# Kernel tuning notes

Measured on AMD Instinct MI355X. Metric: run time of the kernel, lower is better.

## Reference

```python
import jax, jax.numpy as jnp
import numpy as np

B, D, H, O, RH, P = 8192, 784, 2048, 1024, 128, 64
NI = NJ = NK = 4  # input regions / hidden groups / output groups


def _make_groups():
    idx = np.arange(28 * 28).reshape(28, 28)
    input_groups = np.stack([
        idx[:14, :14].ravel(), idx[:14, 14:].ravel(),
        idx[14:, :14].ravel(), idx[14:, 14:].ravel(),
    ]).astype(np.int32)                                   # [4, 196]
    hidden_groups = np.arange(H, dtype=np.int32).reshape(NJ, H // NJ)   # [4, 512]
    output_groups = np.arange(O, dtype=np.int32).reshape(NK, O // NK)   # [4, 256]
    return input_groups, hidden_groups, output_groups


def setup_inputs() -> dict:
    key = jax.random.key(0)
    ks = jax.random.split(key, 9)
    ig, hg, og = _make_groups()
    inp = {
        "x":   jax.random.normal(ks[0], (B, D), jnp.float32),
        "W1":  jax.random.normal(ks[1], (H, D), jnp.float32) / np.sqrt(D),
        "b1":  jax.random.normal(ks[2], (H,), jnp.float32) * 0.01,
        "W2":  jax.random.normal(ks[3], (O, H), jnp.float32) / np.sqrt(H),
        "b2":  jax.random.normal(ks[4], (O,), jnp.float32) * 0.01,
        "Wr1": jax.random.normal(ks[5], (RH, D), jnp.float32) / np.sqrt(D),
        "br1": jax.random.normal(ks[6], (RH,), jnp.float32) * 0.01,
        "Wr2": jax.random.normal(ks[7], (P, RH), jnp.float32) / np.sqrt(RH),
        "br2": jax.random.normal(ks[8], (P,), jnp.float32) * 0.01,
        "input_groups": jnp.asarray(ig),
        "hidden_groups": jnp.asarray(hg),
        "output_groups": jnp.asarray(og),
        "top_k": 8,
    }
    return inp


def reference(x, W1, b1, W2, b2, Wr1, br1, Wr2, br2,
              input_groups, hidden_groups, output_groups, top_k):
    # --- router MLP (eval mode: dropout = identity, no routing noise) ---
    h_r = jax.nn.relu(x @ Wr1.T + br1)
    scores = h_r @ Wr2.T + br2                      # [B, P]
    probs = jax.nn.softmax(scores, axis=-1)         # temperature = 1.0

    # --- top-k pathway selection + renormalization ---
    top_vals, top_idx = jax.lax.top_k(probs, top_k)
    bsz = x.shape[0]
    mask = jnp.zeros_like(probs).at[jnp.arange(bsz)[:, None], top_idx].set(top_vals)
    wts = mask / (mask.sum(axis=-1, keepdims=True) + 1e-8)
    wts4 = wts.reshape(bsz, NI, NJ, NK)             # pathway_idx = i*16 + j*4 + k

    # --- gather pathway sub-blocks ---
    x_reg = x[:, input_groups]                      # [B, I, 196]
    # W1g[i, j] = W1[hidden_groups[j]][:, input_groups[i]] -> [I, J, 512, 196]
    W1g = W1[hidden_groups[None, :, :, None], input_groups[:, None, None, :]]
    b1g = b1[hidden_groups]                         # [J, 512]
    # W2g[j, k] = W2[output_groups[k]][:, hidden_groups[j]] -> [J, K, 256, 512]
    W2g = W2[output_groups[None, :, :, None], hidden_groups[:, None, None, :]]
    b2g = b2[output_groups]                         # [K, 256]

    # --- pathway computation (exact erf GELU, as torch F.gelu default) ---
    hidden = jax.nn.gelu(
        jnp.einsum('bin,ijhn->ijbh', x_reg, W1g) + b1g[None, :, None, :],
        approximate=False)                          # [I, J, B, 512]
    # weighted pathway outputs, contracted over i, j, h without materializing
    # the full [I, J, K, B, 256] tensor
    out_main = jnp.einsum('ijbh,jkoh,bijk->bko', hidden, W2g, wts4)  # [B, K, 256]
    wsum = wts4.sum(axis=(1, 2))                    # [B, K] (bias weighted per pathway)
    out_blocks = out_main + wsum[:, :, None] * b2g[None]

    out = jnp.zeros((bsz, O), x.dtype).at[:, output_groups].add(out_blocks)
    return out
```

## Files before the change

### kernel.cpp

```cpp
#include <hip/hip_runtime.h>
#include <hip/hip_bf16.h>
#include <hip/hip_fp16.h>

#define B_  8192
#define D_  784
#define H_  2048
#define O_  1024
#define RH_ 128
#define P_  64
#define KP  224
#define KC  196

typedef __attribute__((ext_vector_type(8))) short short8;
typedef __attribute__((ext_vector_type(4))) float f32x4;

__device__ inline float bf2f(unsigned short u) {
  union { unsigned int i; float f; } v; v.i = ((unsigned int)u) << 16; return v.f;
}
__device__ inline unsigned short f2bf(float f) {
  __hip_bfloat16 h = __float2bfloat16(f);
  return *reinterpret_cast<unsigned short*>(&h);
}
__device__ inline unsigned short f2h(float f) {
  __half h = __float2half(f);
  return *reinterpret_cast<unsigned short*>(&h);
}
__device__ inline float h2f(unsigned short u) {
  __half h = *reinterpret_cast<__half*>(&u);
  return __half2float(h);
}
__device__ inline float erf_fast(float x) {
  float ax = fabsf(x);
  float t = 1.0f / (1.0f + 0.3275911f * ax);
  float p = ((((1.061405429f * t - 1.453152027f) * t + 1.421413741f) * t
              - 0.284496736f) * t + 0.254829592f) * t;
  float y = 1.0f - p * __expf(-ax * ax);
  return x < 0.f ? -y : y;
}
__device__ inline float gelu_exact(float v) {
  return 0.5f * v * (1.0f + erf_fast(v * 0.70710678118654752f));
}

__device__ inline void gload_lds16(const void* g, void* l) {
  __builtin_amdgcn_global_load_lds((const __attribute__((address_space(1))) void*)g,
                                   (__attribute__((address_space(3))) void*)l, 16, 0, 0);
}

__device__ inline void gemm128_bt(const unsigned short* __restrict__ A,
                                  const unsigned short* __restrict__ Bm,
                                  int K, unsigned short* smem, f32x4 acc[4][4]) {
  const int t = threadIdx.x;
  const int w = t >> 6, l = t & 63;
  const int wr = (w >> 1) * 64, wc = (w & 1) * 64;
  const int lr = l & 15;
  const int swr = (lr >> 1) & 3;
  const int s_orig = (t & 3) ^ ((t >> 3) & 3);
  const size_t srcOff = (size_t)(t >> 2) * K + s_orig * 8;
  const unsigned short* gA = A + srcOff;
  const unsigned short* gB = Bm + srcOff;
  char* lds = (char*)smem;
  char* ldsT = lds + t * 16;
  const int arow = (wr + lr) * 64 + (((l >> 4) ^ swr) * 16);
  const int brow = 8192 + (wc + lr) * 64 + (((l >> 4) ^ swr) * 16);
  const size_t halfA = (size_t)64 * K;
  for (int kt = 0; kt < K; kt += 32) {
    gload_lds16(gA + kt,         ldsT);
    gload_lds16(gA + kt + halfA, ldsT + 4096);
    gload_lds16(gB + kt,         ldsT + 8192);
    gload_lds16(gB + kt + halfA, ldsT + 12288);
    __syncthreads();
    short8 af[4], bfr[4];
#pragma unroll
    for (int f = 0; f < 4; ++f) {
      af[f]  = *(const short8*)(lds + arow + f * 1024);
      bfr[f] = *(const short8*)(lds + brow + f * 1024);
    }
#pragma unroll
    for (int fm = 0; fm < 4; ++fm)
#pragma unroll
      for (int fn = 0; fn < 4; ++fn)
        acc[fm][fn] = __builtin_amdgcn_mfma_f32_16x16x32_bf16(af[fm], bfr[fn], acc[fm][fn], 0, 0, 0);
    __syncthreads();
  }
}

__global__ void k_prep(const float* __restrict__ x, const float* __restrict__ W1,
                       const float* __restrict__ W2, const int* __restrict__ ig,
                       unsigned short* __restrict__ xreg, unsigned short* __restrict__ w1g,
                       unsigned short* __restrict__ w2b) {
  const size_t N1 = (size_t)4 * B_ * KP;
  const size_t N2 = (size_t)4 * H_ * KP;
  const size_t N3 = (size_t)O_ * H_;
  const size_t TOT = N1 + N2 + N3;
  for (size_t idx = (size_t)blockIdx.x * blockDim.x + threadIdx.x; idx < TOT;
       idx += (size_t)gridDim.x * blockDim.x) {
    if (idx < N1) {
      int n = (int)(idx % KP); size_t r = idx / KP;
      int b = (int)(r % B_); int i = (int)(r / B_);
      float v = (n < 196) ? x[(size_t)b * D_ + ig[i * 196 + n]] : 0.f;
      xreg[idx] = f2bf(v);
    } else if (idx < N1 + N2) {
      size_t q = idx - N1;
      int n = (int)(q % KP); size_t r = q / KP;
      int h = (int)(r % H_); int i = (int)(r / H_);
      float v = (n < 196) ? W1[(size_t)h * D_ + ig[i * 196 + n]] : 0.f;
      w1g[q] = f2bf(v);
    } else {
      size_t q = idx - N1 - N2;
      w2b[q] = f2bf(W2[q]);
    }
  }
}

__global__ __launch_bounds__(256) void k_r1s(const float* __restrict__ x,
    const float* __restrict__ Wr1, const float* __restrict__ br1,
    float* __restrict__ hrp) {
  __shared__ float As[64][33];
  __shared__ float Bs[64][33];
  const int b0 = blockIdx.x * 64;
  const int h0 = blockIdx.y * 64;
  const int kb = blockIdx.z * KC;
  const int kend = kb + KC;
  const int t = threadIdx.x;
  const int srow = t >> 2;
  const int scol = (t & 3) * 8;
  const int ty = t >> 4, tx = t & 15;
  float acc[4][4];
#pragma unroll
  for (int i = 0; i < 4; ++i)
#pragma unroll
    for (int j = 0; j < 4; ++j) acc[i][j] = 0.f;
  const float* gA = x   + (size_t)(b0 + srow) * D_;
  const float* gB = Wr1 + (size_t)(h0 + srow) * D_;
  for (int k0 = kb; k0 < kend; k0 += 32) {
    float4 a0 = (k0 + scol + 4  <= kend) ? *(const float4*)(gA + k0 + scol)     : float4{0,0,0,0};
    float4 a1 = (k0 + scol + 8  <= kend) ? *(const float4*)(gA + k0 + scol + 4) : float4{0,0,0,0};
    float4 w0 = (k0 + scol + 4  <= kend) ? *(const float4*)(gB + k0 + scol)     : float4{0,0,0,0};
    float4 w1 = (k0 + scol + 8  <= kend) ? *(const float4*)(gB + k0 + scol + 4) : float4{0,0,0,0};
    __syncthreads();
    *(float4*)&As[srow][scol]     = a0;
    *(float4*)&As[srow][scol + 4] = a1;
    *(float4*)&Bs[srow][scol]     = w0;
    *(float4*)&Bs[srow][scol + 4] = w1;
    __syncthreads();
#pragma unroll
    for (int kk = 0; kk < 8; ++kk) {
      float4 a4[4], b4[4];
#pragma unroll
      for (int i = 0; i < 4; ++i) a4[i] = *(const float4*)&As[ty * 4 + i][kk * 4];
#pragma unroll
      for (int j = 0; j < 4; ++j) b4[j] = *(const float4*)&Bs[tx * 4 + j][kk * 4];
#pragma unroll
      for (int i = 0; i < 4; ++i)
#pragma unroll
        for (int j = 0; j < 4; ++j)
          acc[i][j] += a4[i].x * b4[j].x + a4[i].y * b4[j].y +
                       a4[i].z * b4[j].z + a4[i].w * b4[j].w;
    }
  }
  float* hz = hrp + (size_t)blockIdx.z * B_ * RH_;
#pragma unroll
  for (int j = 0; j < 4; ++j) {
    const int h = h0 + tx * 4 + j;
    const float bias = (blockIdx.z == 0) ? br1[h] : 0.f;
#pragma unroll
    for (int i = 0; i < 4; ++i)
      hz[(size_t)(b0 + ty * 4 + i) * RH_ + h] = acc[i][j] + bias;
  }
}

#define R2S 32
__global__ __launch_bounds__(256) void k_r2(const float* __restrict__ hrp,
    const float* __restrict__ Wr2, const float* __restrict__ br2,
    float* __restrict__ wts, float* __restrict__ wsum) {
  __shared__ float Ws[64][130];
  __shared__ float hs[R2S][128];
  const int s0 = blockIdx.x * R2S;
  const int t = threadIdx.x;
  for (int idx = t; idx < 2048; idx += 256) {
    int r = idx >> 5, c = (idx & 31) * 4;
    *(float4*)&Ws[r][c] = *(const float4*)(Wr2 + (size_t)r * RH_ + c);
  }
  for (int idx = t; idx < R2S * 32; idx += 256) {
    int r = idx >> 5, c = (idx & 31) * 4;
    const size_t off = (size_t)(s0 + r) * RH_ + c;
    float4 p0 = *(const float4*)(hrp + off);
    float4 p1 = *(const float4*)(hrp + (size_t)1 * B_ * RH_ + off);
    float4 p2 = *(const float4*)(hrp + (size_t)2 * B_ * RH_ + off);
    float4 p3 = *(const float4*)(hrp + (size_t)3 * B_ * RH_ + off);
    float4 s;
    s.x = fmaxf(p0.x + p1.x + p2.x + p3.x, 0.f);
    s.y = fmaxf(p0.y + p1.y + p2.y + p3.y, 0.f);
    s.z = fmaxf(p0.z + p1.z + p2.z + p3.z, 0.f);
    s.w = fmaxf(p0.w + p1.w + p2.w + p3.w, 0.f);
    *(float4*)&hs[r][c] = s;
  }
  __syncthreads();
  const int w = t >> 6, p = t & 63;
  const float wb2 = br2[p];
  for (int si = 0; si < R2S / 4; ++si) {
    const int sl = w * (R2S / 4) + si;
    float sc = wb2;
#pragma unroll
    for (int kk = 0; kk < 32; ++kk) {
      float4 h4 = *(const float4*)&hs[sl][kk * 4];
      float4 w4 = *(const float4*)&Ws[p][kk * 4];
      sc += h4.x * w4.x + h4.y * w4.y + h4.z * w4.z + h4.w * w4.w;
    }
    float m = sc;
#pragma unroll
    for (int o = 32; o; o >>= 1) m = fmaxf(m, __shfl_xor(m, o));
    float e = __expf(sc - m);
    float Z = e;
#pragma unroll
    for (int o = 32; o; o >>= 1) Z += __shfl_xor(Z, o);
    bool sel = false;
    float ssum = 0.f;
    for (int it = 0; it < 8; ++it) {
      float v = sel ? -1.f : e;
      float vm = v;
#pragma unroll
      for (int o = 32; o; o >>= 1) vm = fmaxf(vm, __shfl_xor(vm, o));
      unsigned long long mask = __ballot(!sel && v == vm);
      int first = __ffsll((long long)mask) - 1;
      if (p == first) sel = true;
      ssum += vm;
    }
    const float dn = 1.0f / (ssum + 1e-8f * Z);
    const float wv = sel ? e * dn : 0.f;
    wts[(size_t)(s0 + sl) * 64 + p] = wv;
    float part = wv;
#pragma unroll
    for (int o = 4; o < 64; o <<= 1) part += __shfl_xor(part, o);
    if (p < 4) wsum[(size_t)(s0 + sl) * 4 + p] = part;
  }
}

__global__ __launch_bounds__(256) void k_l1(const unsigned short* __restrict__ xreg,
    const unsigned short* __restrict__ w1g, const float* __restrict__ b1,
    unsigned short* __restrict__ hid16) {
  __shared__ __align__(128) unsigned short smem[8192];
  const int mt = blockIdx.x, nt = blockIdx.y, iq = blockIdx.z;
  const unsigned short* A  = xreg + ((size_t)iq * B_ + mt * 128) * KP;
  const unsigned short* Bm = w1g + ((size_t)iq * H_ + nt * 128) * KP;
  f32x4 acc[4][4];
#pragma unroll
  for (int a = 0; a < 4; ++a)
#pragma unroll
    for (int b = 0; b < 4; ++b) acc[a][b] = (f32x4){0.f, 0.f, 0.f, 0.f};
  gemm128_bt(A, Bm, KP, smem, acc);
  const int t = threadIdx.x, w = t >> 6, l = t & 63;
  const int rbase = mt * 128 + (w >> 1) * 64 + (l >> 4) * 4;
  const int cbase = nt * 128 + (w & 1) * 64 + (l & 15);
#pragma unroll
  for (int fn = 0; fn < 4; ++fn) {
    const int n = cbase + fn * 16;
    const float bias = b1[n];
#pragma unroll
    for (int fm = 0; fm < 4; ++fm)
#pragma unroll
      for (int r = 0; r < 4; ++r) {
        const int m = rbase + fm * 16 + r;
        hid16[((size_t)iq * B_ + m) * H_ + n] = f2h(acc[fm][fn][r] + bias);
      }
  }
}

__global__ __launch_bounds__(256) void k_combine(unsigned short* __restrict__ hid,
                                                 const float* __restrict__ wts) {
  const int b = blockIdx.x;
  const int n = threadIdx.x * 8;
  const int j = n >> 9;
  const float* wb = wts + (size_t)b * 64;
  float g[4][8];
#pragma unroll
  for (int i = 0; i < 4; ++i) {
    short8 raw = *(const short8*)(hid + ((size_t)i * B_ + b) * H_ + n);
#pragma unroll
    for (int e = 0; e < 8; ++e) g[i][e] = gelu_exact(h2f((unsigned short)raw[e]));
  }
  short8 outv[4];
#pragma unroll
  for (int k = 0; k < 4; ++k) {
    const float w0 = wb[0 + j * 4 + k], w1 = wb[16 + j * 4 + k];
    const float w2 = wb[32 + j * 4 + k], w3 = wb[48 + j * 4 + k];
#pragma unroll
    for (int e = 0; e < 8; ++e) {
      float sv = g[0][e] * w0 + g[1][e] * w1 + g[2][e] * w2 + g[3][e] * w3;
      outv[k][e] = (short)f2bf(sv);
    }
  }
#pragma unroll
  for (int k = 0; k < 4; ++k)
    *(short8*)(hid + ((size_t)k * B_ + b) * H_ + n) = outv[k];
}

__global__ __launch_bounds__(256) void k_l2(const unsigned short* __restrict__ G,
    const unsigned short* __restrict__ w2b, const float* __restrict__ b2,
    const float* __restrict__ wsum, float* __restrict__ out) {
  __shared__ __align__(128) unsigned short smem[8192];
  const int mt = blockIdx.x, nt = blockIdx.y, k = blockIdx.z;
  const unsigned short* A  = G + ((size_t)k * B_ + mt * 128) * H_;
  const unsigned short* Bm = w2b + ((size_t)(k * 256 + nt * 128)) * H_;
  f32x4 acc[4][4];
#pragma unroll
  for (int a = 0; a < 4; ++a)
#pragma unroll
    for (int b = 0; b < 4; ++b) acc[a][b] = (f32x4){0.f, 0.f, 0.f, 0.f};
  gemm128_bt(A, Bm, H_, smem, acc);
  const int t = threadIdx.x, w = t >> 6, l = t & 63;
  const int rbase = mt * 128 + (w >> 1) * 64 + (l >> 4) * 4;
  const int cb = nt * 128 + (w & 1) * 64 + (l & 15);
#pragma unroll
  for (int fn = 0; fn < 4; ++fn) {
    const int ncol = k * 256 + cb + fn * 16;
    const float bias = b2[ncol];
#pragma unroll
    for (int fm = 0; fm < 4; ++fm)
#pragma unroll
      for (int r = 0; r < 4; ++r) {
        const int m = rbase + fm * 16 + r;
        out[(size_t)m * O_ + ncol] = acc[fm][fn][r] + wsum[m * 4 + k] * bias;
      }
  }
}

extern "C" void kernel_launch(void* const* d_in, const int* in_sizes, int n_in,
                              void* d_out, int out_size, void* d_ws, size_t ws_size,
                              hipStream_t stream) {
  const float* x   = (const float*)d_in[0];
  const float* W1  = (const float*)d_in[1];
  const float* b1  = (const float*)d_in[2];
  const float* W2  = (const float*)d_in[3];
  const float* b2  = (const float*)d_in[4];
  const float* Wr1 = (const float*)d_in[5];
  const float* br1 = (const float*)d_in[6];
  const float* Wr2 = (const float*)d_in[7];
  const float* br2 = (const float*)d_in[8];
  const int*   ig  = (const int*)d_in[9];
  float* out = (float*)d_out;
  char* ws = (char*)d_ws;
  unsigned short* xreg = (unsigned short*)(ws);
  unsigned short* w1g  = (unsigned short*)(ws + 14680064);
  unsigned short* w2b  = (unsigned short*)(ws + 18350080);
  float*          wts  = (float*)(ws + 22544384);
  float*          wsum = (float*)(ws + 24641536);
  unsigned short* hid  = (unsigned short*)(ws + 24772608);
  float*          hrp  = (float*)(ws + 24772608);

  k_prep<<<dim3(2048), dim3(256), 0, stream>>>(x, W1, W2, ig, xreg, w1g, w2b);
  k_r1s<<<dim3(B_ / 64, RH_ / 64, 4), dim3(256), 0, stream>>>(x, Wr1, br1, hrp);
  k_r2<<<dim3(B_ / R2S), dim3(256), 0, stream>>>(hrp, Wr2, br2, wts, wsum);
  k_l1<<<dim3(B_ / 128, H_ / 128, 4), dim3(256), 0, stream>>>(xreg, w1g, b1, hid);
  k_combine<<<dim3(B_), dim3(256), 0, stream>>>(hid, wts);
  k_l2<<<dim3(B_ / 128, 2, 4), dim3(256), 0, stream>>>(hid, w2b, b2, wsum, out);
}
```

Before: 253.5 us.

## Skip inactive (input-region, hidden-group) pathways in layer-1 GEMM via compacted row lists

Adds a compaction kernel that builds, for each (i,j) pair, a list of batch rows whose top-k routing weights are nonzero. The layer-1 GEMM then gathers only those rows, scatters its results back, and exits early for tiles beyond the active count. The combine kernel also skips reading and GELU for inactive i. The lists live temporarily in the output buffer, and the extra launch plus gathered loads add overhead.

```diff
diff --git a/kernel.cpp b/kernel.cpp
--- a/kernel.cpp
+++ b/kernel.cpp
@@ -46,28 +46,23 @@
                                    (__attribute__((address_space(3))) void*)l, 16, 0, 0);
 }
 
-__device__ inline void gemm128_bt(const unsigned short* __restrict__ A,
-                                  const unsigned short* __restrict__ Bm,
-                                  int K, unsigned short* smem, f32x4 acc[4][4]) {
+__device__ inline void gemm128_g(const unsigned short* gA0, const unsigned short* gA1,
+                                 const unsigned short* gB0, const unsigned short* gB1,
+                                 int K, unsigned short* smem, f32x4 acc[4][4]) {
   const int t = threadIdx.x;
   const int w = t >> 6, l = t & 63;
   const int wr = (w >> 1) * 64, wc = (w & 1) * 64;
   const int lr = l & 15;
   const int swr = (lr >> 1) & 3;
-  const int s_orig = (t & 3) ^ ((t >> 3) & 3);
-  const size_t srcOff = (size_t)(t >> 2) * K + s_orig * 8;
-  const unsigned short* gA = A + srcOff;
-  const unsigned short* gB = Bm + srcOff;
   char* lds = (char*)smem;
   char* ldsT = lds + t * 16;
   const int arow = (wr + lr) * 64 + (((l >> 4) ^ swr) * 16);
   const int brow = 8192 + (wc + lr) * 64 + (((l >> 4) ^ swr) * 16);
-  const size_t halfA = (size_t)64 * K;
   for (int kt = 0; kt < K; kt += 32) {
-    gload_lds16(gA + kt,         ldsT);
-    gload_lds16(gA + kt + halfA, ldsT + 4096);
-    gload_lds16(gB + kt,         ldsT + 8192);
-    gload_lds16(gB + kt + halfA, ldsT + 12288);
+    gload_lds16(gA0 + kt, ldsT);
+    gload_lds16(gA1 + kt, ldsT + 4096);
+    gload_lds16(gB0 + kt, ldsT + 8192);
+    gload_lds16(gB1 + kt, ldsT + 12288);
     __syncthreads();
     short8 af[4], bfr[4];
 #pragma unroll
@@ -82,6 +77,16 @@
         acc[fm][fn] = __builtin_amdgcn_mfma_f32_16x16x32_bf16(af[fm], bfr[fn], acc[fm][fn], 0, 0, 0);
     __syncthreads();
   }
+}
+
+__device__ inline void gemm128_bt(const unsigned short* __restrict__ A,
+                                  const unsigned short* __restrict__ Bm,
+                                  int K, unsigned short* smem, f32x4 acc[4][4]) {
+  const int t = threadIdx.x;
+  const int s_orig = (t & 3) ^ ((t >> 3) & 3);
+  const size_t srcOff = (size_t)(t >> 2) * K + s_orig * 8;
+  const size_t halfA = (size_t)64 * K;
+  gemm128_g(A + srcOff, A + srcOff + halfA, Bm + srcOff, Bm + srcOff + halfA, K, smem, acc);
 }
 
 __global__ void k_prep(const float* __restrict__ x, const float* __restrict__ W1,
@@ -236,22 +241,70 @@
   }
 }
 
-__global__ __launch_bounds__(256) void k_l1(const unsigned short* __restrict__ xreg,
+__global__ __launch_bounds__(256) void k_compact(const float* __restrict__ wts,
+                                                 int* __restrict__ lists,
+                                                 int* __restrict__ counts) {
+  __shared__ int wcnt[4];
+  __shared__ int sbase;
+  const int ij = blockIdx.x;
+  const int i = ij >> 2, jj = ij & 3;
+  const int t = threadIdx.x;
+  const int wid = t >> 6, lane = t & 63;
+  if (t == 0) sbase = 0;
+  __syncthreads();
+  for (int b0 = 0; b0 < B_; b0 += 256) {
+    const int b = b0 + t;
+    const float4 w = *(const float4*)(wts + (size_t)b * 64 + i * 16 + jj * 4);
+    const bool act = (w.x != 0.f) || (w.y != 0.f) || (w.z != 0.f) || (w.w != 0.f);
+    const unsigned long long m = __ballot(act);
+    if (lane == 0) wcnt[wid] = __popcll(m);
+    __syncthreads();
+    int off = sbase;
+    const int tot = wcnt[0] + wcnt[1] + wcnt[2] + wcnt[3];
+    for (int q = 0; q < wid; ++q) off += wcnt[q];
+    if (act)
+      lists[(size_t)ij * B_ + off + __popcll(m & ((1ULL << lane) - 1ULL))] = b;
+    __syncthreads();
+    if (t == 0) sbase += tot;
+  }
+  __syncthreads();
+  if (t == 0) counts[ij] = sbase;
+}
+
+__global__ __launch_bounds__(256) void k_l1g(const unsigned short* __restrict__ xreg,
     const unsigned short* __restrict__ w1g, const float* __restrict__ b1,
+    const int* __restrict__ lists, const int* __restrict__ counts,
     unsigned short* __restrict__ hid16) {
+  const int mt = blockIdx.x, nt = blockIdx.y, iq = blockIdx.z;
+  const int ij = iq * 4 + (nt >> 2);
+  const int count = counts[ij];
+  if (mt * 128 >= count) return;
   __shared__ __align__(128) unsigned short smem[8192];
-  const int mt = blockIdx.x, nt = blockIdx.y, iq = blockIdx.z;
-  const unsigned short* A  = xreg + ((size_t)iq * B_ + mt * 128) * KP;
-  const unsigned short* Bm = w1g + ((size_t)iq * H_ + nt * 128) * KP;
+  __shared__ int rows[128];
+  const int t = threadIdx.x;
+  const int* list = lists + (size_t)ij * B_;
+  if (t < 128) {
+    int rl = mt * 128 + t;
+    rows[t] = list[rl < count ? rl : count - 1];
+  }
+  __syncthreads();
+  const int s_orig = (t & 3) ^ ((t >> 3) & 3);
+  const int scol = s_orig * 8;
+  const int r0 = rows[t >> 2], r1 = rows[(t >> 2) + 64];
+  const unsigned short* gA0 = xreg + ((size_t)iq * B_ + r0) * KP + scol;
+  const unsigned short* gA1 = xreg + ((size_t)iq * B_ + r1) * KP + scol;
+  const unsigned short* gB0 = w1g + ((size_t)(iq * H_ + nt * 128) + (t >> 2)) * KP + scol;
+  const unsigned short* gB1 = gB0 + (size_t)64 * KP;
   f32x4 acc[4][4];
 #pragma unroll
   for (int a = 0; a < 4; ++a)
 #pragma unroll
     for (int b = 0; b < 4; ++b) acc[a][b] = (f32x4){0.f, 0.f, 0.f, 0.f};
-  gemm128_bt(A, Bm, KP, smem, acc);
-  const int t = threadIdx.x, w = t >> 6, l = t & 63;
-  const int rbase = mt * 128 + (w >> 1) * 64 + (l >> 4) * 4;
+  gemm128_g(gA0, gA1, gB0, gB1, KP, smem, acc);
+  const int w = t >> 6, l = t & 63;
+  const int rloc0 = (w >> 1) * 64 + (l >> 4) * 4;
   const int cbase = nt * 128 + (w & 1) * 64 + (l & 15);
+  const int mlim = count - mt * 128;
 #pragma unroll
   for (int fn = 0; fn < 4; ++fn) {
     const int n = cbase + fn * 16;
@@ -260,8 +313,9 @@
     for (int fm = 0; fm < 4; ++fm)
 #pragma unroll
       for (int r = 0; r < 4; ++r) {
-        const int m = rbase + fm * 16 + r;
-        hid16[((size_t)iq * B_ + m) * H_ + n] = f2h(acc[fm][fn][r] + bias);
+        const int rl = rloc0 + fm * 16 + r;
+        if (rl < mlim)
+          hid16[((size_t)iq * B_ + rows[rl]) * H_ + n] = f2h(acc[fm][fn][r] + bias);
       }
   }
 }
@@ -271,28 +325,34 @@
   const int b = blockIdx.x;
   const int n = threadIdx.x * 8;
   const int j = n >> 9;
-  const float* wb = wts + (size_t)b * 64;
-  float g[4][8];
+  const float* wb = wts + (size_t)b * 64 + j * 4;
+  float acc[4][8];
+#pragma unroll
+  for (int k = 0; k < 4; ++k)
+#pragma unroll
+    for (int e = 0; e < 8; ++e) acc[k][e] = 0.f;
 #pragma unroll
   for (int i = 0; i < 4; ++i) {
-    short8 raw = *(const short8*)(hid + ((size_t)i * B_ + b) * H_ + n);
-#pragma unroll
-    for (int e = 0; e < 8; ++e) g[i][e] = gelu_exact(h2f((unsigned short)raw[e]));
-  }
-  short8 outv[4];
+    const float4 w4 = *(const float4*)(wb + i * 16);
+    if (w4.x != 0.f || w4.y != 0.f || w4.z != 0.f || w4.w != 0.f) {
+      short8 raw = *(const short8*)(hid + ((size_t)i * B_ + b) * H_ + n);
+#pragma unroll
+      for (int e = 0; e < 8; ++e) {
+        float g = gelu_exact(h2f((unsigned short)raw[e]));
+        acc[0][e] += g * w4.x;
+        acc[1][e] += g * w4.y;
+        acc[2][e] += g * w4.z;
+        acc[3][e] += g * w4.w;
+      }
+    }
+  }
 #pragma unroll
   for (int k = 0; k < 4; ++k) {
-    const float w0 = wb[0 + j * 4 + k], w1 = wb[16 + j * 4 + k];
-    const float w2 = wb[32 + j * 4 + k], w3 = wb[48 + j * 4 + k];
-#pragma unroll
-    for (int e = 0; e < 8; ++e) {
-      float sv = g[0][e] * w0 + g[1][e] * w1 + g[2][e] * w2 + g[3][e] * w3;
-      outv[k][e] = (short)f2bf(sv);
-    }
-  }
-#pragma unroll
-  for (int k = 0; k < 4; ++k)
-    *(short8*)(hid + ((size_t)k * B_ + b) * H_ + n) = outv[k];
+    short8 outv;
+#pragma unroll
+    for (int e = 0; e < 8; ++e) outv[e] = (short)f2bf(acc[k][e]);
+    *(short8*)(hid + ((size_t)k * B_ + b) * H_ + n) = outv;
+  }
 }
 
 __global__ __launch_bounds__(256) void k_l2(const unsigned short* __restrict__ G,
@@ -347,11 +407,14 @@
   float*          wsum = (float*)(ws + 24641536);
   unsigned short* hid  = (unsigned short*)(ws + 24772608);
   float*          hrp  = (float*)(ws + 24772608);
+  int*            lists  = (int*)d_out;
+  int*            counts = lists + 16 * B_;
 
   k_prep<<<dim3(2048), dim3(256), 0, stream>>>(x, W1, W2, ig, xreg, w1g, w2b);
   k_r1s<<<dim3(B_ / 64, RH_ / 64, 4), dim3(256), 0, stream>>>(x, Wr1, br1, hrp);
   k_r2<<<dim3(B_ / R2S), dim3(256), 0, stream>>>(hrp, Wr2, br2, wts, wsum);
-  k_l1<<<dim3(B_ / 128, H_ / 128, 4), dim3(256), 0, stream>>>(xreg, w1g, b1, hid);
+  k_compact<<<dim3(16), dim3(256), 0, stream>>>(wts, lists, counts);
+  k_l1g<<<dim3(B_ / 128, H_ / 128, 4), dim3(256), 0, stream>>>(xreg, w1g, b1, lists, counts, hid);
   k_combine<<<dim3(B_), dim3(256), 0, stream>>>(hid, wts);
   k_l2<<<dim3(B_ / 128, 2, 4), dim3(256), 0, stream>>>(hid, w2b, b2, wsum, out);
 }
```

Measured after the change: 265.1 us. 1.05x slower.
